# Performance work log

Hardware: AMD Instinct MI355X
Metric: run time of the kernel (lower is better)

## Reference

```python
import jax, jax.numpy as jnp
import numpy as np

N = 200000          # graph_size (stalk rows)
H = 128             # hidden_channels
NNZ = 3200000       # Laplacian nnz (avg degree 16)
K = 15              # polynomial degree (poly_layers_K)
LAMBDA_MAX = 2.0    # normalised Laplacian -> analytic lambda_max


def setup_inputs() -> dict:
    key = jax.random.key(0)
    ks = jax.random.split(key, 6)
    x = jax.random.normal(ks[0], (N, H), dtype=jnp.float32)
    vals = jax.random.normal(ks[1], (NNZ,), dtype=jnp.float32)
    poly_logits = jax.random.normal(ks[2], (K + 1,), dtype=jnp.float32)
    hp_alpha = jax.random.normal(ks[3], (), dtype=jnp.float32)
    edge_row = jax.random.randint(ks[4], (NNZ,), 0, N, dtype=jnp.int64)
    edge_col = jax.random.randint(ks[5], (NNZ,), 0, N, dtype=jnp.int64)
    return {"x": x, "vals": vals, "poly_logits": poly_logits,
            "hp_alpha": hp_alpha, "edge_row": edge_row, "edge_col": edge_col}


def reference(x, vals, poly_logits, hp_alpha, edge_row, edge_col):
    n = x.shape[0]

    def spmm(v):  # (n,h) -> (n,h), sparse L @ v in COO form
        return jax.ops.segment_sum(vals[:, None] * v[edge_col], edge_row,
                                   num_segments=n)

    def Lhat(v):  # L_hat = (2/lambda_max) L - I
        return (2.0 / LAMBDA_MAX) * spmm(v) - v

    w = jax.nn.softmax(poly_logits)  # mixture over Chebyshev T_0..T_K

    # Chebyshev Type-1 recurrence: T_{k+1} = 2 L_hat T_k - T_{k-1}
    T0 = x
    T1 = Lhat(x)
    out = w[0] * T0 + w[1] * T1

    def step(carry, wk):
        T0, T1, out = carry
        Tk1 = 2.0 * Lhat(T1) - T0
        return (T1, Tk1, out + wk * Tk1), None

    (_, _, px), _ = jax.lax.scan(step, (T0, T1, out), w[2:])

    # high-pass term: x - (1/lambda_max) L x
    hp = x - spmm(x) / LAMBDA_MAX
    return -px + hp_alpha * hp
```

## Files before the change

### kernel.cpp

```cpp
#include <hip/hip_runtime.h>
#include <math.h>

#define N_NODES 200000
#define H_CH    128
#define GRP     64
#define NNZ_E   3200000
#define K_DEG   15

#define EPB     4096
#define BSHIFT  9
#define NBUCK   391
#define BCAP    9216

__global__ void softmax_k(const float* __restrict__ logits, float* __restrict__ w) {
    if (threadIdx.x == 0) {
        float m = -1e30f;
        for (int i = 0; i <= K_DEG; ++i) m = fmaxf(m, logits[i]);
        float e[K_DEG + 1];
        float s = 0.f;
        for (int i = 0; i <= K_DEG; ++i) { e[i] = expf(logits[i] - m); s += e[i]; }
        float inv = 1.0f / s;
        for (int i = 0; i <= K_DEG; ++i) w[i] = e[i] * inv;
    }
}

__global__ __launch_bounds__(256) void bucketA_k(
    const int* __restrict__ row, const int* __restrict__ col,
    const float* __restrict__ vals, int* __restrict__ counts,
    int* __restrict__ gfill, uint2* __restrict__ stag, int nnz) {
    __shared__ int cnt[NBUCK];
    __shared__ int excl[NBUCK];
    __shared__ int gbase[NBUCK];
    __shared__ int sm[256];
    __shared__ uint2 sstag[EPB];
    __shared__ unsigned short sb[EPB];

    int tid = threadIdx.x;
    int base = blockIdx.x * EPB;

    for (int t = tid; t < NBUCK; t += 256) cnt[t] = 0;
    __syncthreads();

    int r[16], c[16], b[16];
    float v[16];
#pragma unroll
    for (int j = 0; j < 16; ++j) {
        int i = base + j * 256 + tid;
        if (i < nnz) {
            r[j] = row[i]; c[j] = col[i]; v[j] = vals[i];
            b[j] = r[j] >> BSHIFT;
            atomicAdd(&cnt[b[j]], 1);
            atomicAdd(&counts[r[j]], 1);
        } else {
            b[j] = -1;
        }
    }
    __syncthreads();

    {
        int b0 = 2 * tid, b1 = 2 * tid + 1;
        int c0 = (b0 < NBUCK) ? cnt[b0] : 0;
        int c1 = (b1 < NBUCK) ? cnt[b1] : 0;
        int pair = c0 + c1;
        sm[tid] = pair;
        __syncthreads();
        int incl = pair;
        for (int off = 1; off < 256; off <<= 1) {
            int tv = (tid >= off) ? sm[tid - off] : 0;
            __syncthreads();
            incl += tv;
            sm[tid] = incl;
            __syncthreads();
        }
        int pexcl = incl - pair;
        if (b0 < NBUCK) excl[b0] = pexcl;
        if (b1 < NBUCK) excl[b1] = pexcl + c0;
    }
    __syncthreads();

    for (int t = tid; t < NBUCK; t += 256) {
        int cb = cnt[t];
        gbase[t] = (cb > 0) ? atomicAdd(&gfill[t], cb) : 0;
    }
    __syncthreads();
    for (int t = tid; t < NBUCK; t += 256) cnt[t] = excl[t];
    __syncthreads();

#pragma unroll
    for (int j = 0; j < 16; ++j) {
        if (b[j] >= 0) {
            int p = atomicAdd(&cnt[b[j]], 1);
            sstag[p] = make_uint2(((unsigned)(r[j] & 511) << 18) | (unsigned)c[j],
                                  __float_as_uint(v[j]));
            sb[p] = (unsigned short)b[j];
        }
    }
    __syncthreads();

    int tot = nnz - base; if (tot > EPB) tot = EPB;
    for (int i = tid; i < tot; i += 256) {
        int bb = sb[i];
        size_t gp = (size_t)bb * BCAP + gbase[bb] + (i - excl[bb]);
        stag[gp] = sstag[i];
    }
}

__global__ void scan1_k(const int* __restrict__ counts, int* __restrict__ out,
                        int* __restrict__ partials, int n) {
    __shared__ int sm[256];
    int tbase = blockIdx.x * 2048 + threadIdx.x * 8;
    int v[8];
    int tsum = 0;
#pragma unroll
    for (int j = 0; j < 8; ++j) {
        int i = tbase + j;
        int c = (i < n) ? counts[i] : 0;
        v[j] = tsum;
        tsum += c;
    }
    sm[threadIdx.x] = tsum;
    __syncthreads();
    int incl = tsum;
    for (int off = 1; off < 256; off <<= 1) {
        int t = (threadIdx.x >= (unsigned)off) ? sm[threadIdx.x - off] : 0;
        __syncthreads();
        incl += t;
        sm[threadIdx.x] = incl;
        __syncthreads();
    }
    int texcl = incl - tsum;
    if (threadIdx.x == 255) partials[blockIdx.x] = incl;
#pragma unroll
    for (int j = 0; j < 8; ++j) {
        int i = tbase + j;
        if (i < n) out[i] = texcl + v[j];
    }
}

__global__ void scan2_k(int* partials, int nb, int* row_ptr, int n, int total) {
    __shared__ int sm[128];
    int v = (threadIdx.x < (unsigned)nb) ? partials[threadIdx.x] : 0;
    sm[threadIdx.x] = v;
    __syncthreads();
    int incl = v;
    for (int off = 1; off < 128; off <<= 1) {
        int t = (threadIdx.x >= (unsigned)off) ? sm[threadIdx.x - off] : 0;
        __syncthreads();
        incl += t;
        sm[threadIdx.x] = incl;
        __syncthreads();
    }
    if (threadIdx.x < (unsigned)nb) partials[threadIdx.x] = incl - v;
    if (threadIdx.x == 0) row_ptr[n] = total;
}

__global__ void scan3_k(int* __restrict__ row_ptr, const int* __restrict__ partials,
                        int* __restrict__ fill, int n) {
    int off = partials[blockIdx.x];
    int tbase = blockIdx.x * 2048 + threadIdx.x * 8;
#pragma unroll
    for (int j = 0; j < 8; ++j) {
        int i = tbase + j;
        if (i < n) {
            int v = row_ptr[i] + off;
            row_ptr[i] = v;
            fill[i] = v;
        }
    }
}

__global__ __launch_bounds__(256) void bucketB_k(
    const uint2* __restrict__ stag, const int* __restrict__ gfill,
    int* __restrict__ fill, int2* __restrict__ csr) {
    int b = blockIdx.x;
    int n = gfill[b];
    const uint2* s = stag + (size_t)b * BCAP;
    for (int i = threadIdx.x; i < n; i += 256) {
        uint2 e = s[i];
        int rl = (int)(e.x >> 18);
        int cc = (int)(e.x & 0x3FFFF);
        int rr = (b << BSHIFT) | rl;
        int p = atomicAdd(&fill[rr], 1);
        int2 cv;
        cv.x = cc;
        cv.y = (int)e.y;
        csr[p] = cv;
    }
}

__global__ __launch_bounds__(256) void first_k(
    const int* __restrict__ rp, const int2* __restrict__ csr,
    const float* __restrict__ x, float* __restrict__ T1g, float* __restrict__ out,
    const float* __restrict__ w, const float* __restrict__ alpha_p, int goff) {
    int wid = blockIdx.x * 4 + (threadIdx.x >> 6);
    int r = __builtin_amdgcn_readfirstlane(wid);
    if (r >= N_NODES) return;
    int lane = threadIdx.x & 63;
    const float* base = x + goff + lane;
    int e0 = rp[r], e1 = rp[r + 1];
    float a0 = 0.f, a1 = 0.f, a2 = 0.f, a3 = 0.f;
    int e = e0;
    for (; e + 4 <= e1; e += 4) {
        int2 cv0 = csr[e], cv1 = csr[e + 1], cv2 = csr[e + 2], cv3 = csr[e + 3];
        a0 = fmaf(__int_as_float(cv0.y), base[(size_t)cv0.x * H_CH], a0);
        a1 = fmaf(__int_as_float(cv1.y), base[(size_t)cv1.x * H_CH], a1);
        a2 = fmaf(__int_as_float(cv2.y), base[(size_t)cv2.x * H_CH], a2);
        a3 = fmaf(__int_as_float(cv3.y), base[(size_t)cv3.x * H_CH], a3);
    }
    for (; e < e1; ++e) {
        int2 cv = csr[e];
        a0 = fmaf(__int_as_float(cv.y), base[(size_t)cv.x * H_CH], a0);
    }
    float s = (a0 + a1) + (a2 + a3);
    size_t idxg = (size_t)r * GRP + lane;
    size_t idxf = (size_t)r * H_CH + goff + lane;
    float xr = x[idxf];
    float w0 = w[0], w1 = w[1], al = alpha_p[0];
    float t1 = s - xr;
    float o = -(w0 * xr + w1 * t1) + al * (xr - 0.5f * s);
    T1g[idxg] = t1;
    __builtin_nontemporal_store(o, &out[idxf]);
}

__global__ __launch_bounds__(256) void cheb_k(
    const int* __restrict__ rp, const int2* __restrict__ csr,
    const float* __restrict__ Tcur, const float* TprevBase, int tprevStride,
    float* Tnext, float* __restrict__ out,
    const float* __restrict__ w, int k, int goff) {
    int wid = blockIdx.x * 4 + (threadIdx.x >> 6);
    int r = __builtin_amdgcn_readfirstlane(wid);
    if (r >= N_NODES) return;
    int lane = threadIdx.x & 63;
    const float* base = Tcur + lane;
    int e0 = rp[r], e1 = rp[r + 1];
    float a0 = 0.f, a1 = 0.f, a2 = 0.f, a3 = 0.f;
    int e = e0;
    for (; e + 4 <= e1; e += 4) {
        int2 cv0 = csr[e], cv1 = csr[e + 1], cv2 = csr[e + 2], cv3 = csr[e + 3];
        a0 = fmaf(__int_as_float(cv0.y), base[(size_t)cv0.x * GRP], a0);
        a1 = fmaf(__int_as_float(cv1.y), base[(size_t)cv1.x * GRP], a1);
        a2 = fmaf(__int_as_float(cv2.y), base[(size_t)cv2.x * GRP], a2);
        a3 = fmaf(__int_as_float(cv3.y), base[(size_t)cv3.x * GRP], a3);
    }
    for (; e < e1; ++e) {
        int2 cv = csr[e];
        a0 = fmaf(__int_as_float(cv.y), base[(size_t)cv.x * GRP], a0);
    }
    float s = (a0 + a1) + (a2 + a3);
    size_t idxg = (size_t)r * GRP + lane;
    size_t idxf = (size_t)r * H_CH + goff + lane;
    float tc = Tcur[idxg];
    float tp = __builtin_nontemporal_load(&TprevBase[(size_t)r * tprevStride + lane]);
    float wk = w[k];
    float tn = 2.0f * (s - tc) - tp;
    float o = __builtin_nontemporal_load(&out[idxf]);
    o -= wk * tn;
    __builtin_nontemporal_store(o, &out[idxf]);
    Tnext[idxg] = tn;
}

extern "C" void kernel_launch(void* const* d_in, const int* in_sizes, int n_in,
                              void* d_out, int out_size, void* d_ws, size_t ws_size,
                              hipStream_t stream) {
    const float* x      = (const float*)d_in[0];
    const float* vals   = (const float*)d_in[1];
    const float* logits = (const float*)d_in[2];
    const float* alpha  = (const float*)d_in[3];
    const int*   erow   = (const int*)d_in[4];
    const int*   ecol   = (const int*)d_in[5];
    float* out = (float*)d_out;

    const size_t NG = (size_t)N_NODES * GRP;
    float* bufA    = (float*)d_ws;
    float* bufB    = bufA + NG;
    int2*  csr     = (int2*)(bufB + NG);
    uint2* stag    = (uint2*)(csr + NNZ_E);
    int*   row_ptr = (int*)(stag + (size_t)NBUCK * BCAP);
    int*   counts  = row_ptr + (N_NODES + 1);
    int*   gfill   = counts + N_NODES;
    int*   fill    = gfill + NBUCK;
    int*   partials= fill + N_NODES;
    float* w_buf   = (float*)(partials + 128);

    hipMemsetAsync(counts, 0, (N_NODES + NBUCK) * sizeof(int), stream);
    softmax_k<<<1, 64, 0, stream>>>(logits, w_buf);

    int nblkA = (NNZ_E + EPB - 1) / EPB;
    bucketA_k<<<nblkA, 256, 0, stream>>>(erow, ecol, vals, counts, gfill, stag, NNZ_E);

    const int TILE = 2048;
    int nblk = (N_NODES + TILE - 1) / TILE;
    scan1_k<<<nblk, 256, 0, stream>>>(counts, row_ptr, partials, N_NODES);
    scan2_k<<<1, 128, 0, stream>>>(partials, nblk, row_ptr, N_NODES, NNZ_E);
    scan3_k<<<nblk, 256, 0, stream>>>(row_ptr, partials, fill, N_NODES);
    bucketB_k<<<NBUCK, 256, 0, stream>>>(stag, gfill, fill, csr);

    int grid = (N_NODES + 3) / 4;

    for (int g = 0; g < H_CH / GRP; ++g) {
        int goff = g * GRP;
        first_k<<<grid, 256, 0, stream>>>(row_ptr, csr, x, bufB, out, w_buf, alpha, goff);
        cheb_k<<<grid, 256, 0, stream>>>(row_ptr, csr, bufB, x + goff, H_CH, bufA,
                                         out, w_buf, 2, goff);
        float* Tcur = bufA;
        float* Tprev = bufB;
        for (int k = 3; k <= K_DEG; ++k) {
            cheb_k<<<grid, 256, 0, stream>>>(row_ptr, csr, Tcur, Tprev, GRP, Tprev,
                                             out, w_buf, k, goff);
            float* t = Tcur; Tcur = Tprev; Tprev = t;
        }
    }
}
```

Baseline: 4.618 ms.

## Build CSR row pointers per bucket in shared memory, drop global counts scan

Removes the per-edge global atomic row counters and the three-kernel global prefix scan. Row pointers are now built inside each bucket block from a shared-memory histogram and a local scan, offset by a small scan over bucket totals, and edges are placed with shared atomics instead of global ones. Separately, the nontemporal loads and stores on out and Tprev in the Chebyshev kernels become ordinary cached accesses. The preprocessing stage should get cheaper; the cache change could help or hurt the iteration kernels.

```diff
diff --git a/kernel.cpp b/kernel.cpp
--- a/kernel.cpp
+++ b/kernel.cpp
@@ -9,6 +9,7 @@
 
 #define EPB     4096
 #define BSHIFT  9
+#define BROWS   512
 #define NBUCK   391
 #define BCAP    9216
 
@@ -26,7 +27,7 @@
 
 __global__ __launch_bounds__(256) void bucketA_k(
     const int* __restrict__ row, const int* __restrict__ col,
-    const float* __restrict__ vals, int* __restrict__ counts,
+    const float* __restrict__ vals,
     int* __restrict__ gfill, uint2* __restrict__ stag, int nnz) {
     __shared__ int cnt[NBUCK];
     __shared__ int excl[NBUCK];
@@ -50,7 +51,6 @@
             r[j] = row[i]; c[j] = col[i]; v[j] = vals[i];
             b[j] = r[j] >> BSHIFT;
             atomicAdd(&cnt[b[j]], 1);
-            atomicAdd(&counts[r[j]], 1);
         } else {
             b[j] = -1;
         }
@@ -105,84 +105,79 @@
     }
 }
 
-__global__ void scan1_k(const int* __restrict__ counts, int* __restrict__ out,
-                        int* __restrict__ partials, int n) {
+__global__ void scanG_k(const int* __restrict__ gfill, int* __restrict__ bbase,
+                        int* __restrict__ row_ptr) {
     __shared__ int sm[256];
-    int tbase = blockIdx.x * 2048 + threadIdx.x * 8;
-    int v[8];
-    int tsum = 0;
-#pragma unroll
-    for (int j = 0; j < 8; ++j) {
-        int i = tbase + j;
-        int c = (i < n) ? counts[i] : 0;
-        v[j] = tsum;
-        tsum += c;
-    }
-    sm[threadIdx.x] = tsum;
-    __syncthreads();
-    int incl = tsum;
+    int tid = threadIdx.x;
+    int j0 = 2 * tid, j1 = 2 * tid + 1;
+    int c0 = (j0 < NBUCK) ? gfill[j0] : 0;
+    int c1 = (j1 < NBUCK) ? gfill[j1] : 0;
+    int pair = c0 + c1;
+    sm[tid] = pair;
+    __syncthreads();
+    int incl = pair;
     for (int off = 1; off < 256; off <<= 1) {
-        int t = (threadIdx.x >= (unsigned)off) ? sm[threadIdx.x - off] : 0;
+        int t = (tid >= off) ? sm[tid - off] : 0;
         __syncthreads();
         incl += t;
-        sm[threadIdx.x] = incl;
-        __syncthreads();
-    }
-    int texcl = incl - tsum;
-    if (threadIdx.x == 255) partials[blockIdx.x] = incl;
-#pragma unroll
-    for (int j = 0; j < 8; ++j) {
-        int i = tbase + j;
-        if (i < n) out[i] = texcl + v[j];
-    }
-}
-
-__global__ void scan2_k(int* partials, int nb, int* row_ptr, int n, int total) {
-    __shared__ int sm[128];
-    int v = (threadIdx.x < (unsigned)nb) ? partials[threadIdx.x] : 0;
-    sm[threadIdx.x] = v;
-    __syncthreads();
-    int incl = v;
-    for (int off = 1; off < 128; off <<= 1) {
-        int t = (threadIdx.x >= (unsigned)off) ? sm[threadIdx.x - off] : 0;
-        __syncthreads();
-        incl += t;
-        sm[threadIdx.x] = incl;
-        __syncthreads();
-    }
-    if (threadIdx.x < (unsigned)nb) partials[threadIdx.x] = incl - v;
-    if (threadIdx.x == 0) row_ptr[n] = total;
-}
-
-__global__ void scan3_k(int* __restrict__ row_ptr, const int* __restrict__ partials,
-                        int* __restrict__ fill, int n) {
-    int off = partials[blockIdx.x];
-    int tbase = blockIdx.x * 2048 + threadIdx.x * 8;
-#pragma unroll
-    for (int j = 0; j < 8; ++j) {
-        int i = tbase + j;
-        if (i < n) {
-            int v = row_ptr[i] + off;
-            row_ptr[i] = v;
-            fill[i] = v;
-        }
-    }
+        sm[tid] = incl;
+        __syncthreads();
+    }
+    int pexcl = incl - pair;
+    if (j0 < NBUCK) bbase[j0] = pexcl;
+    if (j1 < NBUCK) bbase[j1] = pexcl + c0;
+    if (tid == 0) row_ptr[N_NODES] = NNZ_E;
 }
 
 __global__ __launch_bounds__(256) void bucketB_k(
     const uint2* __restrict__ stag, const int* __restrict__ gfill,
-    int* __restrict__ fill, int2* __restrict__ csr) {
+    const int* __restrict__ bbase, int* __restrict__ row_ptr,
+    int2* __restrict__ csr) {
+    __shared__ int hist[BROWS];
+    __shared__ int lexcl[BROWS];
+    __shared__ int sm[256];
     int b = blockIdx.x;
     int n = gfill[b];
+    int cs = bbase[b];
     const uint2* s = stag + (size_t)b * BCAP;
-    for (int i = threadIdx.x; i < n; i += 256) {
+    int tid = threadIdx.x;
+
+    hist[tid] = 0; hist[tid + 256] = 0;
+    __syncthreads();
+    for (int i = tid; i < n; i += 256)
+        atomicAdd(&hist[s[i].x >> 18], 1);
+    __syncthreads();
+
+    int j0 = 2 * tid, j1 = 2 * tid + 1;
+    int c0 = hist[j0], c1 = hist[j1];
+    int pair = c0 + c1;
+    sm[tid] = pair;
+    __syncthreads();
+    int incl = pair;
+    for (int off = 1; off < 256; off <<= 1) {
+        int t = (tid >= off) ? sm[tid - off] : 0;
+        __syncthreads();
+        incl += t;
+        sm[tid] = incl;
+        __syncthreads();
+    }
+    int pexcl = incl - pair;
+    lexcl[j0] = pexcl;
+    lexcl[j1] = pexcl + c0;
+
+    int rbase = b << BSHIFT;
+    if (rbase + j0 < N_NODES) row_ptr[rbase + j0] = cs + lexcl[j0];
+    if (rbase + j1 < N_NODES) row_ptr[rbase + j1] = cs + lexcl[j1];
+    hist[j0] = lexcl[j0];
+    hist[j1] = lexcl[j1];
+    __syncthreads();
+
+    for (int i = tid; i < n; i += 256) {
         uint2 e = s[i];
         int rl = (int)(e.x >> 18);
-        int cc = (int)(e.x & 0x3FFFF);
-        int rr = (b << BSHIFT) | rl;
-        int p = atomicAdd(&fill[rr], 1);
+        int p = cs + atomicAdd(&hist[rl], 1);
         int2 cv;
-        cv.x = cc;
+        cv.x = (int)(e.x & 0x3FFFF);
         cv.y = (int)e.y;
         csr[p] = cv;
     }
@@ -219,7 +214,7 @@
     float t1 = s - xr;
     float o = -(w0 * xr + w1 * t1) + al * (xr - 0.5f * s);
     T1g[idxg] = t1;
-    __builtin_nontemporal_store(o, &out[idxf]);
+    out[idxf] = o;
 }
 
 __global__ __launch_bounds__(256) void cheb_k(
@@ -250,12 +245,12 @@
     size_t idxg = (size_t)r * GRP + lane;
     size_t idxf = (size_t)r * H_CH + goff + lane;
     float tc = Tcur[idxg];
-    float tp = __builtin_nontemporal_load(&TprevBase[(size_t)r * tprevStride + lane]);
+    float tp = TprevBase[(size_t)r * tprevStride + lane];
     float wk = w[k];
     float tn = 2.0f * (s - tc) - tp;
-    float o = __builtin_nontemporal_load(&out[idxf]);
+    float o = out[idxf];
     o -= wk * tn;
-    __builtin_nontemporal_store(o, &out[idxf]);
+    out[idxf] = o;
     Tnext[idxg] = tn;
 }
 
@@ -276,24 +271,17 @@
     int2*  csr     = (int2*)(bufB + NG);
     uint2* stag    = (uint2*)(csr + NNZ_E);
     int*   row_ptr = (int*)(stag + (size_t)NBUCK * BCAP);
-    int*   counts  = row_ptr + (N_NODES + 1);
-    int*   gfill   = counts + N_NODES;
-    int*   fill    = gfill + NBUCK;
-    int*   partials= fill + N_NODES;
-    float* w_buf   = (float*)(partials + 128);
-
-    hipMemsetAsync(counts, 0, (N_NODES + NBUCK) * sizeof(int), stream);
+    int*   gfill   = row_ptr + (N_NODES + 1);
+    int*   bbase   = gfill + NBUCK;
+    float* w_buf   = (float*)(bbase + NBUCK);
+
+    hipMemsetAsync(gfill, 0, NBUCK * sizeof(int), stream);
     softmax_k<<<1, 64, 0, stream>>>(logits, w_buf);
 
     int nblkA = (NNZ_E + EPB - 1) / EPB;
-    bucketA_k<<<nblkA, 256, 0, stream>>>(erow, ecol, vals, counts, gfill, stag, NNZ_E);
-
-    const int TILE = 2048;
-    int nblk = (N_NODES + TILE - 1) / TILE;
-    scan1_k<<<nblk, 256, 0, stream>>>(counts, row_ptr, partials, N_NODES);
-    scan2_k<<<1, 128, 0, stream>>>(partials, nblk, row_ptr, N_NODES, NNZ_E);
-    scan3_k<<<nblk, 256, 0, stream>>>(row_ptr, partials, fill, N_NODES);
-    bucketB_k<<<NBUCK, 256, 0, stream>>>(stag, gfill, fill, csr);
+    bucketA_k<<<nblkA, 256, 0, stream>>>(erow, ecol, vals, gfill, stag, NNZ_E);
+    scanG_k<<<1, 256, 0, stream>>>(gfill, bbase, row_ptr);
+    bucketB_k<<<NBUCK, 256, 0, stream>>>(stag, gfill, bbase, row_ptr, csr);
 
     int grid = (N_NODES + 3) / 4;
 
```

New measurement: 4.429 ms. -4.1%, faster.
